# Performance work log

Hardware: AMD Instinct MI355X
Metric: run time of the kernel (lower is better)

## Reference

```python
import jax, jax.numpy as jnp
import numpy as np

B, T, C, HS = 8, 4096, 512, 64

def setup_inputs() -> dict:
    key = jax.random.key(0)
    k1, k2, k3, k4 = jax.random.split(key, 4)
    x = jax.random.normal(k1, (B, T, C), dtype=jnp.float32)
    # causal mask (lower-triangular), int32: 1 = keep, 0 = mask out
    mask = jnp.tril(jnp.ones((T, T), dtype=jnp.int32))
    Wk = jax.random.normal(k2, (C, HS), dtype=jnp.float32) * (1.0 / np.sqrt(C))
    Wq = jax.random.normal(k3, (C, HS), dtype=jnp.float32) * (1.0 / np.sqrt(C))
    Wv = jax.random.normal(k4, (C, HS), dtype=jnp.float32) * (1.0 / np.sqrt(C))
    return {"x": x, "mask": mask, "Wk": Wk, "Wq": Wq, "Wv": Wv}

def reference(x, mask, Wk, Wq, Wv):
    # single self-attention head; scale uses C (n_embd), matching the source
    k = jnp.einsum('btc,ch->bth', x, Wk)   # [B,T,HS]
    q = jnp.einsum('btc,ch->bth', x, Wq)
    v = jnp.einsum('btc,ch->bth', x, Wv)
    scale = x.shape[-1] ** -0.5
    wei = jnp.einsum('bth,bsh->bts', q, k) * scale          # [B,T,T]
    wei = jnp.where(mask == 0, jnp.float32(-1e9), wei)
    wei = jax.nn.softmax(wei, axis=-1)
    # dropout is identity in eval mode
    out = jnp.einsum('bts,bsh->bth', wei, v)                # [B,T,HS]
    return out
```

## Files before the change

### kernel.cpp

```cpp
#include <hip/hip_runtime.h>
#include <hip/hip_bf16.h>
#include <stdint.h>

typedef unsigned short u16;
typedef __bf16 bf16x8_t __attribute__((ext_vector_type(8)));
typedef __bf16 bf16x4_t __attribute__((ext_vector_type(4)));
typedef float f32x4_t __attribute__((ext_vector_type(4)));
typedef float f32x8_t __attribute__((ext_vector_type(8)));
typedef float f32x16_t __attribute__((ext_vector_type(16)));
typedef int i32x2_t __attribute__((ext_vector_type(2)));

#define TSEQ 4096
#define CDIM 512
#define HSD  64
#define NBATCH 8

static __device__ __forceinline__ f32x4_t mfma16(bf16x8_t a, bf16x8_t b, f32x4_t c) {
  return __builtin_amdgcn_mfma_f32_16x16x32_bf16(a, b, c, 0, 0, 0);
}
static __device__ __forceinline__ f32x16_t mfma32(bf16x8_t a, bf16x8_t b, f32x16_t c) {
  return __builtin_amdgcn_mfma_f32_32x32x16_bf16(a, b, c, 0, 0, 0);
}

static __device__ __forceinline__ u16 f2bf(float f) {
  union { __bf16 h; u16 s; } v; v.h = (__bf16)f;
  return v.s;
}
static __device__ __forceinline__ float bf2f(u16 h) {
  union { unsigned u; float f; } v; v.u = ((unsigned)h) << 16;
  return v.f;
}
static __device__ __forceinline__ bf16x4_t cvt4(f32x4_t v) {
  return __builtin_convertvector(v, bf16x4_t);
}

static __device__ __forceinline__ void gload16(const void* g, void* l) {
  __builtin_amdgcn_global_load_lds(
      (const __attribute__((address_space(1))) unsigned int*)g,
      (__attribute__((address_space(3))) unsigned int*)l, 16, 0, 0);
}

#define QSCALE (0.044194173824159216f * 1.4426950408889634f)
#define MFIX 32.0f

__global__ __launch_bounds__(256) void repack_w(const float* __restrict__ Wk,
                                                const float* __restrict__ Wq,
                                                const float* __restrict__ Wv,
                                                u16* __restrict__ pw) {
  int i = blockIdx.x * 256 + threadIdx.x;
  int j    = i & 7;
  int l15  = (i >> 3) & 15;
  int quad = (i >> 7) & 3;
  int f    = i >> 9;
  int kc   = f / 12;
  int n12  = f - kc * 12;
  int m    = n12 >> 2;
  int n    = n12 & 3;
  const float* W = (m == 0) ? Wk : ((m == 1) ? Wq : Wv);
  pw[i] = f2bf(W[(kc * 32 + quad * 8 + j) * HSD + n * 16 + l15]);
}

__global__ __launch_bounds__(256, 3) void proj_kernel(const float* __restrict__ x,
                                                      const u16* __restrict__ pw,
                                                      u16* __restrict__ kb,
                                                      u16* __restrict__ qb,
                                                      u16* __restrict__ vb,
                                                      u16* __restrict__ vbT,
                                                      int split) {
  const int tid = threadIdx.x;
  const int lane = tid & 63;
  const int wave = tid >> 6;
  const int l15 = lane & 15, quad = lane >> 4;
  const int bx = (int)blockIdx.x;
  const int rblk = (bx & 7) * 64 + (bx >> 3);
  const int rowLocal = wave * 16 + l15;

  __shared__ __align__(16) char SMEM[24576];
  float (*XS)[2048] = (float (*)[2048])SMEM;
  u16* VtS = (u16*)SMEM;

  const float* xg = x + (size_t)rblk * 64 * CDIM;

  const int xrow = tid >> 3;
  const int xch  = tid & 7;

  f32x4_t acc[12];
#pragma unroll
  for (int n = 0; n < 12; ++n) acc[n] = f32x4_t{0.f, 0.f, 0.f, 0.f};

  auto STAGE = [&](int slot, int kc) {
#pragma unroll
    for (int p = 0; p < 2; ++p) {
      const float* src = xg + (size_t)(p * 32 + xrow) * CDIM + kc * 32 + xch * 4;
      gload16(src, (char*)&XS[slot][0] + p * 4096 + tid * 16);
    }
  };

  STAGE(0, 0);
  STAGE(1, 1);

  const u16* pwl = pw + (size_t)quad * 128 + (size_t)l15 * 8;

  int slot = 0;
#pragma unroll 1
  for (int kc = 0; kc < 16; ++kc) {
    if (kc < 15) asm volatile("s_waitcnt vmcnt(2)" ::: "memory");
    else         asm volatile("s_waitcnt vmcnt(0)" ::: "memory");
    __builtin_amdgcn_s_barrier();

    if (kc + 2 < 16) {
      int s2 = slot + 2; if (s2 >= 3) s2 -= 3;
      STAGE(s2, kc + 2);
    }

    f32x8_t xv = *(const f32x8_t*)&XS[slot][rowLocal * 32 + quad * 8];
    bf16x8_t a = __builtin_convertvector(xv, bf16x8_t);

    const u16* pwk = pwl + (size_t)kc * 6144;
#pragma unroll
    for (int n12 = 0; n12 < 12; ++n12) {
      bf16x8_t b = *(const bf16x8_t*)(pwk + (size_t)n12 * 512);
      acc[n12] = mfma16(a, b, acc[n12]);
    }

    ++slot; if (slot >= 3) slot = 0;
  }

  const int row_base = rblk * 64 + wave * 16 + quad * 4;
#pragma unroll
  for (int n = 0; n < 4; ++n) {
#pragma unroll
    for (int r = 0; r < 4; ++r) {
      kb[(size_t)(row_base + r) * HSD + n * 16 + l15] = f2bf(acc[n][r]);
      qb[(size_t)(row_base + r) * HSD + n * 16 + l15] = f2bf(acc[4 + n][r] * QSCALE);
    }
  }

  if (!split) {
#pragma unroll
    for (int n = 0; n < 4; ++n)
#pragma unroll
      for (int r = 0; r < 4; ++r)
        vb[(size_t)(row_base + r) * HSD + n * 16 + l15] = f2bf(acc[8 + n][r]);
  } else {
    __syncthreads();
#pragma unroll
    for (int n = 0; n < 4; ++n) {
      int h = n * 16 + l15;
      int tl = wave * 16 + quad * 4;
      *(bf16x4_t*)&VtS[h * 72 + tl] = cvt4(acc[8 + n]);
    }
    __syncthreads();
    const int bb = (rblk * 64) >> 12;
    const int t0 = (rblk * 64) & 4095;
#pragma unroll
    for (int it = 0; it < 2; ++it) {
      int g = it * 256 + tid;
      int h = g >> 3;
      int cc = g & 7;
      bf16x8_t vv = *(const bf16x8_t*)&VtS[h * 72 + cc * 8];
      *(bf16x8_t*)&vbT[(size_t)(bb * HSD + h) * TSEQ + t0 + cc * 8] = vv;
    }
  }
}

__global__ __launch_bounds__(256, 4) void attn_part(const u16* __restrict__ qb,
                                                    const u16* __restrict__ kb,
                                                    const u16* __restrict__ vbT,
                                                    u16* __restrict__ pO,
                                                    float* __restrict__ pl) {
  const int b = (int)blockIdx.x & 7;
  const int e = 143 - ((int)blockIdx.y * 18 + ((int)blockIdx.x >> 3));
  int g = 0;
  while (g < 7 && 2 * (g + 1) * (g + 2) <= e) ++g;
  int local = e - 2 * g * (g + 1);
  int qtl = 0;
  while (local >= g + 1) { local -= g + 1; ++qtl; }
  const int qt2 = 4 * g + qtl;
  const int c   = local;

  const int tid = threadIdx.x;
  const int lane = tid & 63;
  const int wave = tid >> 6;
  const int l31 = lane & 31;
  const int h2  = lane >> 5;

  __shared__ __align__(16) char LDS[32768];

  const size_t bo = (size_t)b * TSEQ * HSD;
  const u16* qp = qb + bo;
  const u16* kp = kb + bo;
  const u16* vtp = vbT + (size_t)b * HSD * TSEQ;

  const int qglob = qt2 * 128 + wave * 32 + l31;
  const int wdiag = (qt2 * 128 + wave * 32 + 31) >> 6;

  bf16x8_t qf[4];
#pragma unroll
  for (int kk = 0; kk < 4; ++kk)
    qf[kk] = *(const bf16x8_t*)(qp + (size_t)qglob * HSD + kk * 16 + h2 * 8);

  f32x16_t o0, o1;
#pragma unroll
  for (int i = 0; i < 16; ++i) { o0[i] = 0.f; o1[i] = 0.f; }
  float lsum = 0.f;

  const int st_lo = c * 8;
  const int nt = min(2 * qt2 + 2 - st_lo, 8);

  const int c0 = l31 & 7;
  int A[4];
#pragma unroll
  for (int j = 0; j < 4; ++j) A[j] = l31 * 128 + (((j * 2 + h2) ^ c0) << 4);

  const u16* ksrc[2];
  const u16* vsrc[2];
#pragma unroll
  for (int i = 0; i < 2; ++i) {
    int q = wave * 128 + i * 64 + lane;
    int row = q >> 3, cl = (q & 7) ^ (row & 7);
    ksrc[i] = kp + (size_t)(st_lo * 64 + row) * HSD + cl * 8;
    vsrc[i] = vtp + (size_t)row * TSEQ + st_lo * 64 + cl * 8;
  }

  auto DMA = [&](int t) {
    const int buf = t & 1;
    char* kd = LDS + buf * 8192 + wave * 2048;
    char* vd = LDS + 16384 + buf * 8192 + wave * 2048;
    gload16(ksrc[0] + (size_t)t * 64 * HSD, kd);
    gload16(ksrc[1] + (size_t)t * 64 * HSD, kd + 1024);
    gload16(vsrc[0] + (size_t)t * 64, vd);
    gload16(vsrc[1] + (size_t)t * 64, vd + 1024);
  };

  DMA(0);
  DMA(1);

  auto TILE = [&](int t, int buf) {
    if (t + 1 < nt) asm volatile("s_waitcnt vmcnt(4)" ::: "memory");
    else            asm volatile("s_waitcnt vmcnt(0)" ::: "memory");
    __builtin_amdgcn_s_barrier();

    const int stx = st_lo + t;
    if (stx <= wdiag) {
      const char* kbase = LDS + buf * 8192;
      const char* vbase = LDS + 16384 + buf * 8192;
#pragma unroll
      for (int st2 = 0; st2 < 2; ++st2) {
        f32x16_t s;
#pragma unroll
        for (int i = 0; i < 16; ++i) s[i] = -MFIX;
        __builtin_amdgcn_s_setprio(1);
#pragma unroll
        for (int kk = 0; kk < 4; ++kk) {
          bf16x8_t a = *(const bf16x8_t*)(kbase + st2 * 4096 + A[kk]);
          s = mfma32(a, qf[kk], s);
        }
        __builtin_amdgcn_s_setprio(0);

        if (stx == wdiag) {
#pragma unroll
          for (int i = 0; i < 16; ++i) {
            int sg = stx * 64 + st2 * 32 + 4 * h2 + (i & 3) + 8 * (i >> 2);
            if (sg > qglob) s[i] = -1e9f;
          }
        }

#pragma unroll
        for (int i = 0; i < 16; ++i) s[i] = exp2f(s[i]);
#pragma unroll
        for (int i = 0; i < 16; i += 4)
          lsum += ((s[i] + s[i + 1]) + (s[i + 2] + s[i + 3]));

        union { bf16x4_t v; int d[2]; } X[4];
#pragma unroll
        for (int m = 0; m < 4; ++m) {
          f32x4_t tt;
          tt[0] = s[4 * m]; tt[1] = s[4 * m + 1]; tt[2] = s[4 * m + 2]; tt[3] = s[4 * m + 3];
          X[m].v = cvt4(tt);
        }

        __builtin_amdgcn_s_setprio(1);
#pragma unroll
        for (int kkl = 0; kkl < 2; ++kkl) {
          i32x2_t r0 = __builtin_amdgcn_permlane32_swap(X[2 * kkl].d[0], X[2 * kkl + 1].d[0], false, false);
          i32x2_t r1 = __builtin_amdgcn_permlane32_swap(X[2 * kkl].d[1], X[2 * kkl + 1].d[1], false, false);
          union { bf16x8_t v; int d[4]; } af;
          af.d[0] = r0[0]; af.d[1] = r1[0];
          af.d[2] = r0[1]; af.d[3] = r1[1];
          const int kkg = st2 * 2 + kkl;
          bf16x8_t vf0 = *(const bf16x8_t*)(vbase + A[kkg]);
          bf16x8_t vf1 = *(const bf16x8_t*)(vbase + 4096 + A[kkg]);
          o0 = mfma32(af.v, vf0, o0);
          o1 = mfma32(af.v, vf1, o1);
        }
        __builtin_amdgcn_s_setprio(0);
      }
    }

    __builtin_amdgcn_s_barrier();
    if (t + 2 < nt) DMA(t + 2);
  };

  for (int ip = 0; ip < (nt >> 1); ++ip) {
    TILE(2 * ip, 0);
    TILE(2 * ip + 1, 1);
  }

  lsum += __shfl_xor(lsum, 32);

  const int pidx = (b * 64 + 2 * qt2 + (wave >> 1)) * 8 + c;
  u16* po = pO + (size_t)pidx * 4096;
  float* pm = pl + (size_t)pidx * 64;
#pragma unroll
  for (int i = 0; i < 16; ++i) {
    int rloc = (wave & 1) * 32 + 4 * h2 + (i & 3) + 8 * (i >> 2);
    po[rloc * 64 + l31]      = f2bf(o0[i]);
    po[rloc * 64 + 32 + l31] = f2bf(o1[i]);
  }
  if (lane < 32) pm[(wave & 1) * 32 + lane] = lsum;
}

__global__ __launch_bounds__(256) void attn_combine(const u16* __restrict__ pO,
                                                    const float* __restrict__ pl,
                                                    float* __restrict__ out) {
  const int tid = threadIdx.x;
  const int h2 = tid & 31;
  const int rr = tid >> 5;
  const int rowg = blockIdx.x * 8 + rr;
  const int b = rowg >> 12;
  const int t = rowg & 4095;
  const int qt = t >> 6;
  const int tr = t & 63;
  const int nc = (qt >> 3) + 1;
  const int pbase = (b * 64 + qt) * 8;

  const unsigned* pO32 = (const unsigned*)pO;
  float o0 = 0.f, o1 = 0.f, lsum = 0.f;
  for (int cc = 0; cc < nc; ++cc) {
    lsum += pl[(size_t)(pbase + cc) * 64 + tr];
    unsigned u = pO32[(size_t)(pbase + cc) * 2048 + tr * 32 + h2];
    o0 += bf2f((u16)(u & 0xffffu));
    o1 += bf2f((u16)(u >> 16));
  }
  float2 res;
  res.x = o0 / lsum;
  res.y = o1 / lsum;
  *(float2*)&out[(size_t)rowg * HSD + h2 * 2] = res;
}

__global__ __launch_bounds__(256) void attn_single(const u16* __restrict__ qb,
                                                   const u16* __restrict__ kb,
                                                   const u16* __restrict__ vb,
                                                   float* __restrict__ out) {
  const int qt = (int)gridDim.x - 1 - (int)blockIdx.x;
  const int b = blockIdx.y;
  const int lane = threadIdx.x & 63;
  const int wave = threadIdx.x >> 6;
  const int l15 = lane & 15, quad = lane >> 4;

  __shared__ __align__(16) u16 Ks[64 * 72];
  __shared__ __align__(16) u16 Vt[64 * 72];
  __shared__ __align__(16) u16 Ps[4][16 * 72];

  const size_t bo = (size_t)b * TSEQ * HSD;
  const u16* qp = qb + bo;
  const u16* kp = kb + bo;
  const u16* vp = vb + bo;

  const int qrow0 = qt * 64 + wave * 16;
  bf16x8_t qf0 = *(const bf16x8_t*)(qp + (size_t)(qrow0 + l15) * HSD + quad * 8);
  bf16x8_t qf1 = *(const bf16x8_t*)(qp + (size_t)(qrow0 + l15) * HSD + 32 + quad * 8);

  f32x4_t o[4];
#pragma unroll
  for (int n = 0; n < 4; ++n) o[n] = f32x4_t{0.f, 0.f, 0.f, 0.f};
  float lrow[4] = {0.f, 0.f, 0.f, 0.f};

  const int ldr = threadIdx.x >> 3;
  const int ldc = (threadIdx.x & 7) * 8;

  const f32x4_t sinit = f32x4_t{-MFIX, -MFIX, -MFIX, -MFIX};

  for (int st = 0; st <= qt; ++st) {
    const int s0 = st * 64;
#pragma unroll
    for (int pp = 0; pp < 2; ++pp) {
      int r = ldr + pp * 32;
      bf16x8_t kv = *(const bf16x8_t*)(kp + (size_t)(s0 + r) * HSD + ldc);
      *(bf16x8_t*)&Ks[r * 72 + ldc] = kv;
      bf16x8_t vv = *(const bf16x8_t*)(vp + (size_t)(s0 + r) * HSD + ldc);
      const u16* vu = (const u16*)&vv;
#pragma unroll
      for (int j = 0; j < 8; ++j) Vt[(ldc + j) * 72 + r] = vu[j];
    }
    __syncthreads();

    f32x4_t s[4];
#pragma unroll
    for (int n = 0; n < 4; ++n) {
      bf16x8_t k0 = *(const bf16x8_t*)&Ks[(n * 16 + l15) * 72 + quad * 8];
      bf16x8_t k1 = *(const bf16x8_t*)&Ks[(n * 16 + l15) * 72 + 32 + quad * 8];
      f32x4_t a = sinit;
      a = mfma16(qf0, k0, a);
      a = mfma16(qf1, k1, a);
      s[n] = a;
    }

    if (st == qt) {
#pragma unroll
      for (int n = 0; n < 4; ++n) {
        int sg = s0 + n * 16 + l15;
#pragma unroll
        for (int r = 0; r < 4; ++r) {
          int tg = qrow0 + quad * 4 + r;
          if (sg > tg) s[n][r] = -1e9f;
        }
      }
    }

#pragma unroll
    for (int n = 0; n < 4; ++n)
#pragma unroll
      for (int r = 0; r < 4; ++r) {
        float p = exp2f(s[n][r]);
        s[n][r] = p;
        lrow[r] += p;
      }

    u16* myP = Ps[wave];
#pragma unroll
    for (int n = 0; n < 4; ++n)
#pragma unroll
      for (int r = 0; r < 4; ++r)
        myP[(quad * 4 + r) * 72 + n * 16 + l15] = f2bf(s[n][r]);

    __syncthreads();

#pragma unroll
    for (int kc = 0; kc < 2; ++kc) {
      bf16x8_t pf = *(const bf16x8_t*)&myP[l15 * 72 + kc * 32 + quad * 8];
#pragma unroll
      for (int n = 0; n < 4; ++n) {
        bf16x8_t vf = *(const bf16x8_t*)&Vt[(n * 16 + l15) * 72 + kc * 32 + quad * 8];
        o[n] = mfma16(pf, vf, o[n]);
      }
    }
    __syncthreads();
  }

#pragma unroll
  for (int r = 0; r < 4; ++r) {
    float l = lrow[r];
    l += __shfl_xor(l, 1);
    l += __shfl_xor(l, 2);
    l += __shfl_xor(l, 4);
    l += __shfl_xor(l, 8);
    lrow[r] = l;
  }

#pragma unroll
  for (int n = 0; n < 4; ++n)
#pragma unroll
    for (int r = 0; r < 4; ++r)
      out[bo + (size_t)(qrow0 + quad * 4 + r) * HSD + n * 16 + l15] = o[n][r] / lrow[r];
}

extern "C" void kernel_launch(void* const* d_in, const int* in_sizes, int n_in,
                              void* d_out, int out_size, void* d_ws, size_t ws_size,
                              hipStream_t stream) {
  const float* x  = (const float*)d_in[0];
  const float* Wk = (const float*)d_in[2];
  const float* Wq = (const float*)d_in[3];
  const float* Wv = (const float*)d_in[4];
  float* out = (float*)d_out;

  char* base = (char*)d_ws;
  const size_t KV = (size_t)NBATCH * TSEQ * HSD;
  u16* pw  = (u16*)base;
  u16* kb  = (u16*)(base + (1 << 18));
  u16* qb  = kb + KV;
  u16* vbT = qb + KV;
  u16* pO  = vbT + KV;
  u16* vb  = pO;
  float* pl = (float*)(pO + (size_t)4096 * 4096);
  const size_t need = (size_t)(1 << 18) + 3 * KV * 2
                    + (size_t)4096 * 4096 * 2
                    + (size_t)4096 * 64 * 4;
  const int split = (ws_size >= need) ? 1 : 0;

  hipLaunchKernelGGL(repack_w, dim3(384), dim3(256), 0, stream, Wk, Wq, Wv, pw);
  hipLaunchKernelGGL(proj_kernel, dim3(512), dim3(256), 0, stream, x, pw, kb, qb, vb, vbT, split);
  if (split) {
    hipLaunchKernelGGL(attn_part, dim3(144, NBATCH), dim3(256), 0, stream, qb, kb, vbT, pO, pl);
    hipLaunchKernelGGL(attn_combine, dim3(4096), dim3(256), 0, stream, pO, pl, out);
  } else {
    hipLaunchKernelGGL(attn_single, dim3(64, NBATCH), dim3(256), 0, stream, qb, kb, vb, out);
  }
}
```

Measured before the change: 212.0 us.

## Load x directly from global in projection kernel, dropping LDS triple buffer

Replaces the triple-buffered async LDS staging of x tiles (with waitcnt and barriers) in the QKV projection kernel with direct per-lane 32-byte global loads feeding the MFMA A operand. The loop is unrolled by 2 and the occupancy hint is removed. The goal is to cut LDS traffic, barriers and shared memory footprint. In exchange the global accesses are less coalesced (each lane reads 32 bytes at a 2 KB row stride) and latency hiding now depends on the compiler and occupancy. The projection is a small part of total time next to attention.

```diff
diff --git a/kernel.cpp b/kernel.cpp
--- a/kernel.cpp
+++ b/kernel.cpp
@@ -60,70 +60,40 @@
   pw[i] = f2bf(W[(kc * 32 + quad * 8 + j) * HSD + n * 16 + l15]);
 }
 
-__global__ __launch_bounds__(256, 3) void proj_kernel(const float* __restrict__ x,
-                                                      const u16* __restrict__ pw,
-                                                      u16* __restrict__ kb,
-                                                      u16* __restrict__ qb,
-                                                      u16* __restrict__ vb,
-                                                      u16* __restrict__ vbT,
-                                                      int split) {
+__global__ __launch_bounds__(256) void proj_kernel(const float* __restrict__ x,
+                                                   const u16* __restrict__ pw,
+                                                   u16* __restrict__ kb,
+                                                   u16* __restrict__ qb,
+                                                   u16* __restrict__ vb,
+                                                   u16* __restrict__ vbT,
+                                                   int split) {
   const int tid = threadIdx.x;
   const int lane = tid & 63;
   const int wave = tid >> 6;
   const int l15 = lane & 15, quad = lane >> 4;
   const int bx = (int)blockIdx.x;
   const int rblk = (bx & 7) * 64 + (bx >> 3);
-  const int rowLocal = wave * 16 + l15;
-
-  __shared__ __align__(16) char SMEM[24576];
-  float (*XS)[2048] = (float (*)[2048])SMEM;
-  u16* VtS = (u16*)SMEM;
-
-  const float* xg = x + (size_t)rblk * 64 * CDIM;
-
-  const int xrow = tid >> 3;
-  const int xch  = tid & 7;
+
+  __shared__ __align__(16) u16 VtS[64 * 72];
+
+  const int row = rblk * 64 + wave * 16 + l15;
+  const float* xr = x + (size_t)row * CDIM + quad * 8;
+  const u16* pwl = pw + (size_t)quad * 128 + (size_t)l15 * 8;
 
   f32x4_t acc[12];
 #pragma unroll
   for (int n = 0; n < 12; ++n) acc[n] = f32x4_t{0.f, 0.f, 0.f, 0.f};
 
-  auto STAGE = [&](int slot, int kc) {
-#pragma unroll
-    for (int p = 0; p < 2; ++p) {
-      const float* src = xg + (size_t)(p * 32 + xrow) * CDIM + kc * 32 + xch * 4;
-      gload16(src, (char*)&XS[slot][0] + p * 4096 + tid * 16);
-    }
-  };
-
-  STAGE(0, 0);
-  STAGE(1, 1);
-
-  const u16* pwl = pw + (size_t)quad * 128 + (size_t)l15 * 8;
-
-  int slot = 0;
-#pragma unroll 1
+#pragma unroll 2
   for (int kc = 0; kc < 16; ++kc) {
-    if (kc < 15) asm volatile("s_waitcnt vmcnt(2)" ::: "memory");
-    else         asm volatile("s_waitcnt vmcnt(0)" ::: "memory");
-    __builtin_amdgcn_s_barrier();
-
-    if (kc + 2 < 16) {
-      int s2 = slot + 2; if (s2 >= 3) s2 -= 3;
-      STAGE(s2, kc + 2);
-    }
-
-    f32x8_t xv = *(const f32x8_t*)&XS[slot][rowLocal * 32 + quad * 8];
+    f32x8_t xv = *(const f32x8_t*)(xr + kc * 32);
     bf16x8_t a = __builtin_convertvector(xv, bf16x8_t);
-
     const u16* pwk = pwl + (size_t)kc * 6144;
 #pragma unroll
     for (int n12 = 0; n12 < 12; ++n12) {
       bf16x8_t b = *(const bf16x8_t*)(pwk + (size_t)n12 * 512);
       acc[n12] = mfma16(a, b, acc[n12]);
     }
-
-    ++slot; if (slot >= 3) slot = 0;
   }
 
   const int row_base = rblk * 64 + wave * 16 + quad * 4;
@@ -143,7 +113,6 @@
       for (int r = 0; r < 4; ++r)
         vb[(size_t)(row_base + r) * HSD + n * 16 + l15] = f2bf(acc[8 + n][r]);
   } else {
-    __syncthreads();
 #pragma unroll
     for (int n = 0; n < 4; ++n) {
       int h = n * 16 + l15;
```

Measured after the change: 201.6 us. -4.9%, faster.
